# Optimization experiments

Hardware: AMD Instinct MI355X
Metric: run time of the kernel (lower is better)

The kernel has to match this reference:

```python
import jax, jax.numpy as jnp
import numpy as np

B, C, D, H, W = 4, 64, 32, 64, 64
CH = C // 2


def setup_inputs() -> dict:
    key = jax.random.key(0)
    ks = jax.random.split(key, 9)
    s = 0.05
    return {
        "x": jax.random.normal(ks[0], (B, C, D, H, W), dtype=jnp.float32),
        "wqr": jax.random.normal(ks[1], (1, C), dtype=jnp.float32) * s,
        "wvr": jax.random.normal(ks[2], (CH, C), dtype=jnp.float32) * s,
        "wup": jax.random.normal(ks[3], (C, CH), dtype=jnp.float32) * s,
        "wql": jax.random.normal(ks[4], (CH, C), dtype=jnp.float32) * s,
        "wvl": jax.random.normal(ks[5], (CH, C), dtype=jnp.float32) * s,
        "wsk1": jax.random.normal(ks[6], (CH, C), dtype=jnp.float32) * s,
        "wsk2": jax.random.normal(ks[7], (C, CH), dtype=jnp.float32) * s,
        "wres": jax.random.normal(ks[8], (C, C), dtype=jnp.float32) * s,
    }


def reference(x, wqr, wvr, wup, wql, wvl, wsk1, wsk2, wres):
    b, c, d, h, w = x.shape
    ch = c // 2
    n = d * h * w
    xf = x.reshape(b, c, n)
    # 1x1x1 conv (bias=False) + default mmcv ReLU activation
    conv = lambda Wt, t: jax.nn.relu(jnp.einsum('oc,bcn->bon', Wt, t))

    # ---- spatial (GCNet-style) branch ----
    input_x = conv(wvr, xf)                              # [b,ch,n]
    mask = jax.nn.softmax(conv(wqr, xf)[:, 0], axis=-1)  # [b,n]
    context = jnp.einsum('bcn,bn->bc', input_x, mask)    # [b,ch]
    mu = context.mean(-1, keepdims=True)
    var = context.var(-1, keepdims=True)                 # biased, like F.layer_norm
    ln = (context - mu) / jnp.sqrt(var + 1e-5)
    # conv_up with HSigmoid(bias=3, divisor=6)
    spatial_attn = jnp.clip((jnp.einsum('oc,bc->bo', wup, ln) + 3.0) / 6.0, 0.0, 1.0)  # [b,c]

    # ---- channel branch ----
    g_x = conv(wql, xf)                                  # [b,ch,n]
    avg_x = jax.nn.softmax(g_x.mean(-1), axis=-1)        # [b,ch]
    theta_x = conv(wvl, xf)                              # [b,ch,n]
    channel_attn = jax.nn.sigmoid(jnp.einsum('bc,bcn->bn', avg_x, theta_x))  # [b,n]

    # ---- recombination ----
    sequence = spatial_attn[:, :, None] * channel_attn[:, None, :]           # [b,c,n]
    parallel = jax.nn.softmax(channel_attn[:, None, :] + spatial_attn[:, :, None], axis=-1)

    # ---- SK gating ----
    u = (sequence + parallel).mean(-1)                   # global avg pool -> [b,c]
    a = jax.nn.relu(jnp.einsum('oc,bc->bo', wsk1, u))    # [b,ch]
    a = jax.nn.relu(jnp.einsum('oc,bc->bo', wsk2, a))    # [b,c]
    a = jax.nn.softmax(a, axis=-1)                       # softmax over channels
    sk = sequence * a[:, :, None] + parallel * (1.0 - a[:, :, None])  # [b,c,n]

    # ---- with_self=True path ----
    out = sk.sum(-1)[:, :, None] + conv(wres, xf)        # [b,c,n]
    return out.reshape(b, c, d, h, w)
```

## Files before the change

### kernel.cpp

```cpp
#include <hip/hip_runtime.h>

#define NB 4
#define NC 64
#define NCH 32
#define NPIX 131072

#define O_SUME 0
#define O_CTX  8
#define O_QL   136
#define O_SCA  264
#define O_SA   272
#define O_AVGX 528
#define O_K    656
#define O_WT1  1024
#define WT1_S  68
#define O_WT3  6144
#define O_WT5  8192
#define AF1_OFF 4096u
#define AF3_OFF 14336u
#define AF5_OFF 18432u
#define PB_OFF  32768u
#define PB_F    8192
#define XT_OFF  327680u
#define WS_NEED 67436544u

typedef short bf16x8 __attribute__((ext_vector_type(8)));
typedef float f32x4  __attribute__((ext_vector_type(4)));
typedef unsigned short u16x8 __attribute__((ext_vector_type(8)));

__device__ __forceinline__ float wave_sum64(float v) {
#pragma unroll
    for (int m = 32; m; m >>= 1) v += __shfl_xor(v, m, 64);
    return v;
}
__device__ __forceinline__ float gsum16(float v) {
#pragma unroll
    for (int m = 8; m; m >>= 1) v += __shfl_xor(v, m, 64);
    return v;
}
__device__ __forceinline__ unsigned short f2bf(float f) {
    unsigned u = __float_as_uint(f);
    u += 0x7FFFu + ((u >> 16) & 1u);
    return (unsigned short)(u >> 16);
}


__global__ __launch_bounds__(256) void k_T(
    const float* __restrict__ x, unsigned short* __restrict__ xt,
    const float* __restrict__ wqr, const float* __restrict__ wvr,
    const float* __restrict__ wql, const float* __restrict__ wvl,
    const float* __restrict__ wres, float* __restrict__ ws) {
    if (blockIdx.x == 0 && blockIdx.y == 0) {
        unsigned short* af1 = (unsigned short*)((char*)ws + AF1_OFF);
        unsigned short* af3 = (unsigned short*)((char*)ws + AF3_OFF);
        unsigned short* af5 = (unsigned short*)((char*)ws + AF5_OFF);
        for (int idx = threadIdx.x; idx < 5 * 2 * 64 * 8; idx += 256) {
            int j = idx & 7, lane = (idx >> 3) & 63, s = (idx >> 9) & 1, t = idx >> 10;
            int row = lane & 15, kg = lane >> 4, c = s * 32 + kg * 8 + j;
            float v;
            if (t < 2)      v = wvr[(t * 16 + row) * NC + c];
            else if (t < 4) v = wql[((t - 2) * 16 + row) * NC + c];
            else            v = (row == 0) ? wqr[c] : 0.f;
            af1[idx] = f2bf(v);
        }
        for (int idx = threadIdx.x; idx < 2 * 2 * 64 * 8; idx += 256) {
            int j = idx & 7, lane = (idx >> 3) & 63, s = (idx >> 9) & 1, t = idx >> 10;
            int row = lane & 15, kg = lane >> 4, c = s * 32 + kg * 8 + j;
            af3[idx] = f2bf(wvl[(t * 16 + row) * NC + c]);
        }
        for (int idx = threadIdx.x; idx < 4 * 2 * 64 * 8; idx += 256) {
            int j = idx & 7, lane = (idx >> 3) & 63, s = (idx >> 9) & 1, t = idx >> 10;
            int row = lane & 15, kg = lane >> 4, c = s * 32 + kg * 8 + j;
            af5[idx] = f2bf(wres[(t * 16 + row) * NC + c]);
        }
    }
    const int b = blockIdx.y;
    const int n0 = blockIdx.x * 64;
    __shared__ float lds[64 * 65];
    const int t = threadIdx.x;
    const int c = t >> 2, q = t & 3;
    const float* src = x + (size_t)(b * NC + c) * NPIX + n0;
#pragma unroll
    for (int k = 0; k < 4; ++k) {
        float4 v = *(const float4*)(src + q * 4 + k * 16);
        lds[c * 65 + q * 4 + k * 16 + 0] = v.x;
        lds[c * 65 + q * 4 + k * 16 + 1] = v.y;
        lds[c * 65 + q * 4 + k * 16 + 2] = v.z;
        lds[c * 65 + q * 4 + k * 16 + 3] = v.w;
    }
    __syncthreads();
    const int nl = t >> 2, cq = t & 3;
    u16x8 o0, o1;
#pragma unroll
    for (int i = 0; i < 8; ++i) o0[i] = f2bf(lds[(cq * 16 + i) * 65 + nl]);
#pragma unroll
    for (int i = 0; i < 8; ++i) o1[i] = f2bf(lds[(cq * 16 + 8 + i) * 65 + nl]);
    unsigned short* dst = xt + ((size_t)b * NPIX + n0 + nl) * NC + cq * 16;
    *(u16x8*)(dst) = o0;
    *(u16x8*)(dst + 8) = o1;
}

#define TPW 8
__global__ __launch_bounds__(256) void k_p1(
    const unsigned short* __restrict__ xt, float* __restrict__ ws) {
    const int b = blockIdx.y;
    const int lane = threadIdx.x & 63;
    const int wid = blockIdx.x * 4 + (threadIdx.x >> 6);
    const int col = lane & 15, kg = lane >> 4;
    const unsigned short* af1 = (const unsigned short*)((const char*)ws + AF1_OFF);

    __shared__ float red[65];
    for (int i = threadIdx.x; i < 65; i += 256) red[i] = 0.f;
    __syncthreads();

    bf16x8 A[5][2];
#pragma unroll
    for (int t = 0; t < 5; ++t)
#pragma unroll
        for (int s = 0; s < 2; ++s)
            A[t][s] = *(const bf16x8*)(af1 + ((t * 2 + s) * 64 + lane) * 8);

    float ctx[8], qla[8];
#pragma unroll
    for (int i = 0; i < 8; ++i) { ctx[i] = 0.f; qla[i] = 0.f; }
    float acc_e = 0.f;

    for (int it = 0; it < TPW; ++it) {
        const int n0 = (wid * TPW + it) * 16;
        const unsigned short* xr = xt + ((size_t)b * NPIX + n0 + col) * NC + kg * 8;
        bf16x8 B0 = *(const bf16x8*)(xr);
        bf16x8 B1 = *(const bf16x8*)(xr + 32);

        f32x4 c6 = {0.f, 0.f, 0.f, 0.f};
        c6 = __builtin_amdgcn_mfma_f32_16x16x32_bf16(A[4][0], B0, c6, 0, 0, 0);
        c6 = __builtin_amdgcn_mfma_f32_16x16x32_bf16(A[4][1], B1, c6, 0, 0, 0);
        float e = __expf(fmaxf(c6[0], 0.f));
        e = __shfl(e, col, 64);
        acc_e += e;

        f32x4 c0 = {0.f, 0.f, 0.f, 0.f}, c1 = {0.f, 0.f, 0.f, 0.f};
        c0 = __builtin_amdgcn_mfma_f32_16x16x32_bf16(A[0][0], B0, c0, 0, 0, 0);
        c0 = __builtin_amdgcn_mfma_f32_16x16x32_bf16(A[0][1], B1, c0, 0, 0, 0);
        c1 = __builtin_amdgcn_mfma_f32_16x16x32_bf16(A[1][0], B0, c1, 0, 0, 0);
        c1 = __builtin_amdgcn_mfma_f32_16x16x32_bf16(A[1][1], B1, c1, 0, 0, 0);
#pragma unroll
        for (int r = 0; r < 4; ++r) {
            ctx[r]     += fmaxf(c0[r], 0.f) * e;
            ctx[4 + r] += fmaxf(c1[r], 0.f) * e;
        }
        c0 = f32x4{0.f, 0.f, 0.f, 0.f}; c1 = f32x4{0.f, 0.f, 0.f, 0.f};
        c0 = __builtin_amdgcn_mfma_f32_16x16x32_bf16(A[2][0], B0, c0, 0, 0, 0);
        c0 = __builtin_amdgcn_mfma_f32_16x16x32_bf16(A[2][1], B1, c0, 0, 0, 0);
        c1 = __builtin_amdgcn_mfma_f32_16x16x32_bf16(A[3][0], B0, c1, 0, 0, 0);
        c1 = __builtin_amdgcn_mfma_f32_16x16x32_bf16(A[3][1], B1, c1, 0, 0, 0);
#pragma unroll
        for (int r = 0; r < 4; ++r) {
            qla[r]     += fmaxf(c0[r], 0.f);
            qla[4 + r] += fmaxf(c1[r], 0.f);
        }
    }

    acc_e = wave_sum64(acc_e) * 0.25f;
    if (lane == 0) atomicAdd(&red[64], acc_e);
#pragma unroll
    for (int i = 0; i < 8; ++i) {
        float v = gsum16(ctx[i]);
        float q = gsum16(qla[i]);
        if (col == 0) {
            int ch = (i >> 2) * 16 + kg * 4 + (i & 3);
            atomicAdd(&red[ch], v);
            atomicAdd(&red[32 + ch], q);
        }
    }
    __syncthreads();
    float* pb = ws + PB_F;
    if (threadIdx.x < 65)
        pb[((size_t)b * 65 + threadIdx.x) * 256 + blockIdx.x] = red[threadIdx.x];
}

__global__ __launch_bounds__(256) void k_p2f(
    const float* __restrict__ wup, float* __restrict__ ws) {
    const int b = threadIdx.x >> 6;
    const int lane = threadIdx.x & 63;
    __shared__ float q_s[NB][65];
    __shared__ float ln_s[NB][NCH];
    if (threadIdx.x < NB) ws[O_SCA + threadIdx.x] = 0.f;
    const float* pb = ws + PB_F;
    {
        const float4* p = (const float4*)(pb + ((size_t)b * 65 + lane) * 256);
        float s = 0.f;
        for (int k = 0; k < 64; ++k) { float4 v = p[k]; s += v.x + v.y + v.z + v.w; }
        q_s[b][lane] = s;
        if (lane == 0) {
            const float4* pe = (const float4*)(pb + ((size_t)b * 65 + 64) * 256);
            float se = 0.f;
            for (int k = 0; k < 64; ++k) { float4 v = pe[k]; se += v.x + v.y + v.z + v.w; }
            q_s[b][64] = se;
        }
    }
    __syncthreads();

    float se = q_s[b][64];
    float ctx = (lane < NCH) ? (q_s[b][lane] / se) : 0.f;
    float v = ctx, v2 = ctx * ctx;
#pragma unroll
    for (int m = 16; m; m >>= 1) { v += __shfl_xor(v, m, 64); v2 += __shfl_xor(v2, m, 64); }
    float mu = v / (float)NCH;
    float var = v2 / (float)NCH - mu * mu;
    float lnv = (ctx - mu) * rsqrtf(var + 1e-5f);
    if (lane < NCH) ln_s[b][lane] = lnv;
    __syncthreads();
    float s = 0.f;
#pragma unroll
    for (int ch = 0; ch < NCH; ++ch) s = fmaf(wup[lane * NCH + ch], ln_s[b][ch], s);
    ws[O_SA + b * NC + lane] = fminf(fmaxf((s + 3.f) * (1.f / 6.f), 0.f), 1.f);
    if (lane < NCH) {
        float l = q_s[b][32 + lane] * (1.f / (float)NPIX);
        float mx = l;
#pragma unroll
        for (int m = 16; m; m >>= 1) mx = fmaxf(mx, __shfl_xor(mx, m, 64));
        float e = __expf(l - mx);
        float sm = e;
#pragma unroll
        for (int m = 16; m; m >>= 1) sm += __shfl_xor(sm, m, 64);
        ws[O_AVGX + b * NCH + lane] = e / sm;
    }
}

__global__ __launch_bounds__(256) void k_p3v(
    const unsigned short* __restrict__ xt, float* __restrict__ ws) {
    const int b = blockIdx.y;
    const int lane = threadIdx.x & 63;
    const int wid = blockIdx.x * 4 + (threadIdx.x >> 6);
    const int col = lane & 15, kg = lane >> 4;
    const unsigned short* af3 = (const unsigned short*)((const char*)ws + AF3_OFF);

    __shared__ float red;
    if (threadIdx.x == 0) red = 0.f;
    __syncthreads();

    bf16x8 A[2][2];
#pragma unroll
    for (int t = 0; t < 2; ++t)
#pragma unroll
        for (int s = 0; s < 2; ++s)
            A[t][s] = *(const bf16x8*)(af3 + ((t * 2 + s) * 64 + lane) * 8);
    float ax0[4], ax1[4];
#pragma unroll
    for (int r = 0; r < 4; ++r) {
        ax0[r] = ws[O_AVGX + b * NCH + kg * 4 + r];
        ax1[r] = ws[O_AVGX + b * NCH + 16 + kg * 4 + r];
    }

    float acc = 0.f;
    for (int it = 0; it < TPW; ++it) {
        const int n0 = (wid * TPW + it) * 16;
        const unsigned short* xr = xt + ((size_t)b * NPIX + n0 + col) * NC + kg * 8;
        bf16x8 B0 = *(const bf16x8*)(xr);
        bf16x8 B1 = *(const bf16x8*)(xr + 32);
        f32x4 c0 = {0.f, 0.f, 0.f, 0.f}, c1 = {0.f, 0.f, 0.f, 0.f};
        c0 = __builtin_amdgcn_mfma_f32_16x16x32_bf16(A[0][0], B0, c0, 0, 0, 0);
        c0 = __builtin_amdgcn_mfma_f32_16x16x32_bf16(A[0][1], B1, c0, 0, 0, 0);
        c1 = __builtin_amdgcn_mfma_f32_16x16x32_bf16(A[1][0], B0, c1, 0, 0, 0);
        c1 = __builtin_amdgcn_mfma_f32_16x16x32_bf16(A[1][1], B1, c1, 0, 0, 0);
        float sp = 0.f;
#pragma unroll
        for (int r = 0; r < 4; ++r) {
            sp = fmaf(ax0[r], fmaxf(c0[r], 0.f), sp);
            sp = fmaf(ax1[r], fmaxf(c1[r], 0.f), sp);
        }
        sp += __shfl_xor(sp, 16, 64);
        sp += __shfl_xor(sp, 32, 64);
        acc += 1.f / (1.f + __expf(-sp));
    }
    acc = wave_sum64(acc) * 0.25f;
    if (lane == 0) atomicAdd(&red, acc);
    __syncthreads();
    if (threadIdx.x == 0) atomicAdd(&ws[O_SCA + b], red);
}

__global__ __launch_bounds__(256) void k_p5(
    const unsigned short* __restrict__ xt, const float* __restrict__ ws,
    const float* __restrict__ wsk1, const float* __restrict__ wsk2,
    float* __restrict__ out) {
    const int b = blockIdx.y;
    const int tid = threadIdx.x;
    const int lane = tid & 63;
    const int wid = blockIdx.x * 4 + (tid >> 6);
    const int col = lane & 15, kg = lane >> 4;
    const unsigned short* af5 = (const unsigned short*)((const char*)ws + AF5_OFF);

    __shared__ float u_s[NC];
    __shared__ float a1_s[NCH];
    __shared__ float K_s[NC];

    const float invn = 1.f / (float)NPIX;
    if (tid < NC) {
        float sca = ws[O_SCA + b];
        float sa = ws[O_SA + b * NC + tid];
        u_s[tid] = fmaf(sa, sca * invn, invn);
    }
    __syncthreads();
    if (tid < NCH) {
        float s = 0.f;
#pragma unroll
        for (int c = 0; c < NC; ++c) s = fmaf(wsk1[tid * NC + c], u_s[c], s);
        a1_s[tid] = fmaxf(s, 0.f);
    }
    __syncthreads();
    if (tid < NC) {
        float s2 = 0.f;
#pragma unroll
        for (int ch = 0; ch < NCH; ++ch) s2 = fmaf(wsk2[tid * NCH + ch], a1_s[ch], s2);
        s2 = fmaxf(s2, 0.f);
        float mx = s2;
#pragma unroll
        for (int m = 32; m; m >>= 1) mx = fmaxf(mx, __shfl_xor(mx, m, 64));
        float e = __expf(s2 - mx);
        float sm = e;
#pragma unroll
        for (int m = 32; m; m >>= 1) sm += __shfl_xor(sm, m, 64);
        float a = e / sm;
        float sca = ws[O_SCA + b];
        float sa = ws[O_SA + b * NC + tid];
        K_s[tid] = fmaf(a, sa * sca, 1.f - a);
    }
    __syncthreads();

    bf16x8 A[4][2];
#pragma unroll
    for (int t = 0; t < 4; ++t)
#pragma unroll
        for (int s = 0; s < 2; ++s)
            A[t][s] = *(const bf16x8*)(af5 + ((t * 2 + s) * 64 + lane) * 8);
    float kv[4][4];
#pragma unroll
    for (int t = 0; t < 4; ++t)
#pragma unroll
        for (int r = 0; r < 4; ++r)
            kv[t][r] = K_s[t * 16 + kg * 4 + r];

    for (int it = 0; it < TPW; ++it) {
        const int n0 = (wid * TPW + it) * 16;
        const unsigned short* xr = xt + ((size_t)b * NPIX + n0 + col) * NC + kg * 8;
        bf16x8 B0 = *(const bf16x8*)(xr);
        bf16x8 B1 = *(const bf16x8*)(xr + 32);
#pragma unroll
        for (int t = 0; t < 4; ++t) {
            f32x4 c = {0.f, 0.f, 0.f, 0.f};
            c = __builtin_amdgcn_mfma_f32_16x16x32_bf16(A[t][0], B0, c, 0, 0, 0);
            c = __builtin_amdgcn_mfma_f32_16x16x32_bf16(A[t][1], B1, c, 0, 0, 0);
#pragma unroll
            for (int r = 0; r < 4; ++r) {
                int o = t * 16 + kg * 4 + r;
                out[((size_t)(b * NC + o)) * NPIX + n0 + col] = kv[t][r] + fmaxf(c[r], 0.f);
            }
        }
    }
}

__global__ __launch_bounds__(256) void k_prep(
    const float* __restrict__ wqr, const float* __restrict__ wvr,
    const float* __restrict__ wql, const float* __restrict__ wvl,
    const float* __restrict__ wres, float* __restrict__ ws) {
    for (int i = threadIdx.x; i < NC * WT1_S; i += 256) {
        int c = i / WT1_S, j = i % WT1_S;
        float v = 0.f;
        if (j == 0)       v = wqr[c];
        else if (j <= 32) v = wvr[(j - 1) * NC + c];
        else if (j <= 64) v = wql[(j - 33) * NC + c];
        ws[O_WT1 + i] = v;
    }
    for (int i = threadIdx.x; i < NC * NCH; i += 256) {
        int c = i / NCH, ch = i % NCH;
        ws[O_WT3 + i] = wvl[ch * NC + c];
    }
    for (int i = threadIdx.x; i < NC * NC; i += 256) {
        int c = i / NC, o = i % NC;
        ws[O_WT5 + i] = wres[o * NC + c];
    }
}

__global__ __launch_bounds__(256) void k_pass1(
    const float* __restrict__ x, float* __restrict__ ws) {
    const int b = blockIdx.y;
    const float* xb = x + (size_t)b * NC * NPIX;
    __shared__ float wlds[NC * WT1_S];
    __shared__ float red[1 + 2 * NCH];
    for (int i = threadIdx.x; i < NC * WT1_S; i += 256) wlds[i] = ws[O_WT1 + i];
    for (int i = threadIdx.x; i < 1 + 2 * NCH; i += 256) red[i] = 0.f;
    __syncthreads();
    const int n2 = blockIdx.x * 256 + threadIdx.x;
    float dqr0 = 0.f, dqr1 = 0.f;
    float dv[NCH][2], dq[NCH][2];
#pragma unroll
    for (int i = 0; i < NCH; ++i) { dv[i][0] = dv[i][1] = 0.f; dq[i][0] = dq[i][1] = 0.f; }
    for (int c = 0; c < NC; ++c) {
        const float2 xv = *(const float2*)(xb + (size_t)c * NPIX + 2 * n2);
        const float* wr = wlds + c * WT1_S;
        dqr0 = fmaf(wr[0], xv.x, dqr0);
        dqr1 = fmaf(wr[0], xv.y, dqr1);
#pragma unroll
        for (int ch = 0; ch < NCH; ++ch) {
            const float wv = wr[1 + ch], wq = wr[33 + ch];
            dv[ch][0] = fmaf(wv, xv.x, dv[ch][0]);
            dv[ch][1] = fmaf(wv, xv.y, dv[ch][1]);
            dq[ch][0] = fmaf(wq, xv.x, dq[ch][0]);
            dq[ch][1] = fmaf(wq, xv.y, dq[ch][1]);
        }
    }
    const float e0 = __expf(fmaxf(dqr0, 0.f));
    const float e1 = __expf(fmaxf(dqr1, 0.f));
    float acc_e = wave_sum64(e0 + e1);
    if ((threadIdx.x & 63) == 0) atomicAdd(&red[0], acc_e);
#pragma unroll
    for (int ch = 0; ch < NCH; ++ch) {
        float v = wave_sum64(fmaxf(dv[ch][0], 0.f) * e0 + fmaxf(dv[ch][1], 0.f) * e1);
        float q = wave_sum64(fmaxf(dq[ch][0], 0.f) + fmaxf(dq[ch][1], 0.f));
        if ((threadIdx.x & 63) == 0) { atomicAdd(&red[1 + ch], v); atomicAdd(&red[1 + NCH + ch], q); }
    }
    __syncthreads();
    if (threadIdx.x == 0) atomicAdd(&ws[O_SUME + b], red[0]);
    if (threadIdx.x < NCH) {
        atomicAdd(&ws[O_CTX + b * NCH + threadIdx.x], red[1 + threadIdx.x]);
        atomicAdd(&ws[O_QL  + b * NCH + threadIdx.x], red[1 + NCH + threadIdx.x]);
    }
}

__global__ __launch_bounds__(256) void k_pass2(
    const float* __restrict__ wup, float* __restrict__ ws) {
    const int b = threadIdx.x >> 6;
    const int lane = threadIdx.x & 63;
    __shared__ float ln_s[NB][NCH];
    float se = ws[O_SUME + b];
    float ctx = (lane < NCH) ? (ws[O_CTX + b * NCH + lane] / se) : 0.f;
    float v = ctx, v2 = ctx * ctx;
#pragma unroll
    for (int m = 16; m; m >>= 1) { v += __shfl_xor(v, m, 64); v2 += __shfl_xor(v2, m, 64); }
    float mu = v / (float)NCH;
    float var = v2 / (float)NCH - mu * mu;
    float lnv = (ctx - mu) * rsqrtf(var + 1e-5f);
    if (lane < NCH) ln_s[b][lane] = lnv;
    __syncthreads();
    float s = 0.f;
#pragma unroll
    for (int ch = 0; ch < NCH; ++ch) s = fmaf(wup[lane * NCH + ch], ln_s[b][ch], s);
    ws[O_SA + b * NC + lane] = fminf(fmaxf((s + 3.f) * (1.f / 6.f), 0.f), 1.f);
    if (lane < NCH) {
        float l = ws[O_QL + b * NCH + lane] * (1.f / (float)NPIX);
        float mx = l;
#pragma unroll
        for (int m = 16; m; m >>= 1) mx = fmaxf(mx, __shfl_xor(mx, m, 64));
        float e = __expf(l - mx);
        float sm = e;
#pragma unroll
        for (int m = 16; m; m >>= 1) sm += __shfl_xor(sm, m, 64);
        ws[O_AVGX + b * NCH + lane] = e / sm;
    }
}

__global__ __launch_bounds__(256) void k_pass3(
    const float* __restrict__ x, float* __restrict__ ws) {
    const int b = blockIdx.y;
    const float* xb = x + (size_t)b * NC * NPIX;
    __shared__ float wlds[NC * NCH];
    __shared__ float red;
    for (int i = threadIdx.x; i < NC * NCH; i += 256) wlds[i] = ws[O_WT3 + i];
    if (threadIdx.x == 0) red = 0.f;
    __syncthreads();
    const int n2 = blockIdx.x * 256 + threadIdx.x;
    float dv[NCH][2];
#pragma unroll
    for (int i = 0; i < NCH; ++i) dv[i][0] = dv[i][1] = 0.f;
    for (int c = 0; c < NC; ++c) {
        const float2 xv = *(const float2*)(xb + (size_t)c * NPIX + 2 * n2);
        const float* wr = wlds + c * NCH;
#pragma unroll
        for (int ch = 0; ch < NCH; ++ch) {
            dv[ch][0] = fmaf(wr[ch], xv.x, dv[ch][0]);
            dv[ch][1] = fmaf(wr[ch], xv.y, dv[ch][1]);
        }
    }
    float s0 = 0.f, s1 = 0.f;
#pragma unroll
    for (int ch = 0; ch < NCH; ++ch) {
        const float ax = ws[O_AVGX + b * NCH + ch];
        s0 = fmaf(ax, fmaxf(dv[ch][0], 0.f), s0);
        s1 = fmaf(ax, fmaxf(dv[ch][1], 0.f), s1);
    }
    float acc = wave_sum64(1.f / (1.f + __expf(-s0)) + 1.f / (1.f + __expf(-s1)));
    if ((threadIdx.x & 63) == 0) atomicAdd(&red, acc);
    __syncthreads();
    if (threadIdx.x == 0) atomicAdd(&ws[O_SCA + b], red);
}

__global__ __launch_bounds__(256) void k_pass4(
    const float* __restrict__ wsk1, const float* __restrict__ wsk2,
    float* __restrict__ ws) {
    const int b = threadIdx.x >> 6;
    const int lane = threadIdx.x & 63;
    __shared__ float u_s[NB][NC];
    __shared__ float a1_s[NB][NCH];
    float sca = ws[O_SCA + b];
    float sa = ws[O_SA + b * NC + lane];
    float invn = 1.f / (float)NPIX;
    u_s[b][lane] = fmaf(sa, sca * invn, invn);
    __syncthreads();
    if (lane < NCH) {
        float s = 0.f;
#pragma unroll
        for (int c = 0; c < NC; ++c) s = fmaf(wsk1[lane * NC + c], u_s[b][c], s);
        a1_s[b][lane] = fmaxf(s, 0.f);
    }
    __syncthreads();
    float s2 = 0.f;
#pragma unroll
    for (int ch = 0; ch < NCH; ++ch) s2 = fmaf(wsk2[lane * NCH + ch], a1_s[b][ch], s2);
    s2 = fmaxf(s2, 0.f);
    float mx = s2;
#pragma unroll
    for (int m = 32; m; m >>= 1) mx = fmaxf(mx, __shfl_xor(mx, m, 64));
    float e = __expf(s2 - mx);
    float sm = e;
#pragma unroll
    for (int m = 32; m; m >>= 1) sm += __shfl_xor(sm, m, 64);
    float a = e / sm;
    ws[O_K + b * NC + lane] = fmaf(a, sa * sca, 1.f - a);
}

__global__ __launch_bounds__(256) void k_pass5(
    const float* __restrict__ x, const float* __restrict__ ws,
    float* __restrict__ out) {
    const int b = blockIdx.y;
    const float* xb = x + (size_t)b * NC * NPIX;
    float* ob = out + (size_t)b * NC * NPIX;
    __shared__ float wlds[NC * NC];
    for (int i = threadIdx.x; i < NC * NC; i += 256) wlds[i] = ws[O_WT5 + i];
    __syncthreads();
    const int n2 = blockIdx.x * 256 + threadIdx.x;
    float acc[NC][2];
#pragma unroll
    for (int o = 0; o < NC; ++o) acc[o][0] = acc[o][1] = 0.f;
    for (int c = 0; c < NC; ++c) {
        const float2 xv = *(const float2*)(xb + (size_t)c * NPIX + 2 * n2);
        const float* wr = wlds + c * NC;
#pragma unroll
        for (int o = 0; o < NC; ++o) {
            acc[o][0] = fmaf(wr[o], xv.x, acc[o][0]);
            acc[o][1] = fmaf(wr[o], xv.y, acc[o][1]);
        }
    }
#pragma unroll
    for (int o = 0; o < NC; ++o) {
        const float k = ws[O_K + b * NC + o];
        float2 r;
        r.x = k + fmaxf(acc[o][0], 0.f);
        r.y = k + fmaxf(acc[o][1], 0.f);
        *(float2*)(ob + (size_t)o * NPIX + 2 * n2) = r;
    }
}

extern "C" void kernel_launch(void* const* d_in, const int* in_sizes, int n_in,
                              void* d_out, int out_size, void* d_ws, size_t ws_size,
                              hipStream_t stream) {
    const float* x    = (const float*)d_in[0];
    const float* wqr  = (const float*)d_in[1];
    const float* wvr  = (const float*)d_in[2];
    const float* wup  = (const float*)d_in[3];
    const float* wql  = (const float*)d_in[4];
    const float* wvl  = (const float*)d_in[5];
    const float* wsk1 = (const float*)d_in[6];
    const float* wsk2 = (const float*)d_in[7];
    const float* wres = (const float*)d_in[8];
    float* out = (float*)d_out;
    float* ws  = (float*)d_ws;

    dim3 blk(256);

    if (ws_size >= (size_t)WS_NEED) {
        unsigned short* xt = (unsigned short*)((char*)d_ws + XT_OFF);
        k_T<<<dim3(NPIX / 64, NB), blk, 0, stream>>>(x, xt, wqr, wvr, wql, wvl, wres, ws);
        k_p1<<<dim3(NPIX / (16 * 4 * TPW), NB), blk, 0, stream>>>(xt, ws);
        k_p2f<<<dim3(1), blk, 0, stream>>>(wup, ws);
        k_p3v<<<dim3(NPIX / (16 * 4 * TPW), NB), blk, 0, stream>>>(xt, ws);
        k_p5<<<dim3(NPIX / (16 * 4 * TPW), NB), blk, 0, stream>>>(xt, ws, wsk1, wsk2, out);
    } else {
        hipMemsetAsync(d_ws, 0, 272 * sizeof(float), stream);
        k_prep<<<dim3(1), blk, 0, stream>>>(wqr, wvr, wql, wvl, wres, ws);
        dim3 g(NPIX / (2 * 256), NB);
        k_pass1<<<g, blk, 0, stream>>>(x, ws);
        k_pass2<<<dim3(1), blk, 0, stream>>>(wup, ws);
        k_pass3<<<g, blk, 0, stream>>>(x, ws);
        k_pass4<<<dim3(1), blk, 0, stream>>>(wsk1, wsk2, ws);
        k_pass5<<<g, blk, 0, stream>>>(x, ws, out);
    }
}
```

Baseline: 147.1 us.

## Fuse transpose with first statistics pass and transpose final MFMA output

Merges the fp32-to-bf16 transpose kernel with the first reduction pass, so the statistics MMAs read the tile straight from LDS instead of re-reading the transposed copy from global memory. Per-block partials go to a larger buffer that a new parallel reduction kernel sums before the small finalize kernel. The final residual-conv kernel swaps the MFMA operands so each lane writes a float4 along pixels rather than scattered scalar stores. In exchange, the fused kernel loads weights from global memory in every block and the partial buffer grows.

```diff
diff --git a/kernel.cpp b/kernel.cpp
--- a/kernel.cpp
+++ b/kernel.cpp
@@ -16,13 +16,13 @@
 #define WT1_S  68
 #define O_WT3  6144
 #define O_WT5  8192
-#define AF1_OFF 4096u
 #define AF3_OFF 14336u
 #define AF5_OFF 18432u
 #define PB_OFF  32768u
 #define PB_F    8192
-#define XT_OFF  327680u
-#define WS_NEED 67436544u
+#define NBLK    2048
+#define XT_OFF  2162688u
+#define WS_NEED 69271552u
 
 typedef short bf16x8 __attribute__((ext_vector_type(8)));
 typedef float f32x4  __attribute__((ext_vector_type(4)));
@@ -43,41 +43,45 @@
     u += 0x7FFFu + ((u >> 16) & 1u);
     return (unsigned short)(u >> 16);
 }
-
-
-__global__ __launch_bounds__(256) void k_T(
+__device__ __forceinline__ bf16x8 ld8f(const float* p) {
+    float4 a = *(const float4*)p;
+    float4 c = *(const float4*)(p + 4);
+    bf16x8 r;
+    r[0] = (short)f2bf(a.x); r[1] = (short)f2bf(a.y);
+    r[2] = (short)f2bf(a.z); r[3] = (short)f2bf(a.w);
+    r[4] = (short)f2bf(c.x); r[5] = (short)f2bf(c.y);
+    r[6] = (short)f2bf(c.z); r[7] = (short)f2bf(c.w);
+    return r;
+}
+
+
+__global__ __launch_bounds__(256) void k_Tp1(
     const float* __restrict__ x, unsigned short* __restrict__ xt,
     const float* __restrict__ wqr, const float* __restrict__ wvr,
     const float* __restrict__ wql, const float* __restrict__ wvl,
     const float* __restrict__ wres, float* __restrict__ ws) {
-    if (blockIdx.x == 0 && blockIdx.y == 0) {
-        unsigned short* af1 = (unsigned short*)((char*)ws + AF1_OFF);
+    const int b = blockIdx.y;
+    const int n0 = blockIdx.x * 64;
+    const int t = threadIdx.x;
+    __shared__ float lds[64 * 65];
+    __shared__ float red[65];
+
+    if (blockIdx.x == 0 && b == 0) {
         unsigned short* af3 = (unsigned short*)((char*)ws + AF3_OFF);
         unsigned short* af5 = (unsigned short*)((char*)ws + AF5_OFF);
-        for (int idx = threadIdx.x; idx < 5 * 2 * 64 * 8; idx += 256) {
-            int j = idx & 7, lane = (idx >> 3) & 63, s = (idx >> 9) & 1, t = idx >> 10;
+        for (int idx = t; idx < 2 * 2 * 64 * 8; idx += 256) {
+            int j = idx & 7, lane = (idx >> 3) & 63, s = (idx >> 9) & 1, tt = idx >> 10;
             int row = lane & 15, kg = lane >> 4, c = s * 32 + kg * 8 + j;
-            float v;
-            if (t < 2)      v = wvr[(t * 16 + row) * NC + c];
-            else if (t < 4) v = wql[((t - 2) * 16 + row) * NC + c];
-            else            v = (row == 0) ? wqr[c] : 0.f;
-            af1[idx] = f2bf(v);
-        }
-        for (int idx = threadIdx.x; idx < 2 * 2 * 64 * 8; idx += 256) {
-            int j = idx & 7, lane = (idx >> 3) & 63, s = (idx >> 9) & 1, t = idx >> 10;
+            af3[idx] = f2bf(wvl[(tt * 16 + row) * NC + c]);
+        }
+        for (int idx = t; idx < 4 * 2 * 64 * 8; idx += 256) {
+            int j = idx & 7, lane = (idx >> 3) & 63, s = (idx >> 9) & 1, tt = idx >> 10;
             int row = lane & 15, kg = lane >> 4, c = s * 32 + kg * 8 + j;
-            af3[idx] = f2bf(wvl[(t * 16 + row) * NC + c]);
-        }
-        for (int idx = threadIdx.x; idx < 4 * 2 * 64 * 8; idx += 256) {
-            int j = idx & 7, lane = (idx >> 3) & 63, s = (idx >> 9) & 1, t = idx >> 10;
-            int row = lane & 15, kg = lane >> 4, c = s * 32 + kg * 8 + j;
-            af5[idx] = f2bf(wres[(t * 16 + row) * NC + c]);
-        }
-    }
-    const int b = blockIdx.y;
-    const int n0 = blockIdx.x * 64;
-    __shared__ float lds[64 * 65];
-    const int t = threadIdx.x;
+            af5[idx] = f2bf(wres[(tt * 16 + row) * NC + c]);
+        }
+    }
+    for (int i = t; i < 65; i += 256) red[i] = 0.f;
+
     const int c = t >> 2, q = t & 3;
     const float* src = x + (size_t)(b * NC + c) * NPIX + n0;
 #pragma unroll
@@ -89,144 +93,110 @@
         lds[c * 65 + q * 4 + k * 16 + 3] = v.w;
     }
     __syncthreads();
+
     const int nl = t >> 2, cq = t & 3;
-    u16x8 o0, o1;
-#pragma unroll
-    for (int i = 0; i < 8; ++i) o0[i] = f2bf(lds[(cq * 16 + i) * 65 + nl]);
-#pragma unroll
-    for (int i = 0; i < 8; ++i) o1[i] = f2bf(lds[(cq * 16 + 8 + i) * 65 + nl]);
-    unsigned short* dst = xt + ((size_t)b * NPIX + n0 + nl) * NC + cq * 16;
-    *(u16x8*)(dst) = o0;
-    *(u16x8*)(dst + 8) = o1;
-}
-
-#define TPW 8
-__global__ __launch_bounds__(256) void k_p1(
-    const unsigned short* __restrict__ xt, float* __restrict__ ws) {
-    const int b = blockIdx.y;
-    const int lane = threadIdx.x & 63;
-    const int wid = blockIdx.x * 4 + (threadIdx.x >> 6);
+    {
+        u16x8 o0, o1;
+#pragma unroll
+        for (int i = 0; i < 8; ++i) o0[i] = f2bf(lds[(cq * 16 + i) * 65 + nl]);
+#pragma unroll
+        for (int i = 0; i < 8; ++i) o1[i] = f2bf(lds[(cq * 16 + 8 + i) * 65 + nl]);
+        unsigned short* dst = xt + ((size_t)b * NPIX + n0 + nl) * NC + cq * 16;
+        *(u16x8*)(dst) = o0;
+        *(u16x8*)(dst + 8) = o1;
+    }
+
+    const int lane = t & 63, w = t >> 6;
     const int col = lane & 15, kg = lane >> 4;
-    const unsigned short* af1 = (const unsigned short*)((const char*)ws + AF1_OFF);
-
-    __shared__ float red[65];
-    for (int i = threadIdx.x; i < 65; i += 256) red[i] = 0.f;
-    __syncthreads();
-
-    bf16x8 A[5][2];
-#pragma unroll
-    for (int t = 0; t < 5; ++t)
-#pragma unroll
-        for (int s = 0; s < 2; ++s)
-            A[t][s] = *(const bf16x8*)(af1 + ((t * 2 + s) * 64 + lane) * 8);
-
-    float ctx[8], qla[8];
-#pragma unroll
-    for (int i = 0; i < 8; ++i) { ctx[i] = 0.f; qla[i] = 0.f; }
-    float acc_e = 0.f;
-
-    for (int it = 0; it < TPW; ++it) {
-        const int n0 = (wid * TPW + it) * 16;
-        const unsigned short* xr = xt + ((size_t)b * NPIX + n0 + col) * NC + kg * 8;
-        bf16x8 B0 = *(const bf16x8*)(xr);
-        bf16x8 B1 = *(const bf16x8*)(xr + 32);
-
-        f32x4 c6 = {0.f, 0.f, 0.f, 0.f};
-        c6 = __builtin_amdgcn_mfma_f32_16x16x32_bf16(A[4][0], B0, c6, 0, 0, 0);
-        c6 = __builtin_amdgcn_mfma_f32_16x16x32_bf16(A[4][1], B1, c6, 0, 0, 0);
-        float e = __expf(fmaxf(c6[0], 0.f));
-        e = __shfl(e, col, 64);
-        acc_e += e;
-
-        f32x4 c0 = {0.f, 0.f, 0.f, 0.f}, c1 = {0.f, 0.f, 0.f, 0.f};
-        c0 = __builtin_amdgcn_mfma_f32_16x16x32_bf16(A[0][0], B0, c0, 0, 0, 0);
-        c0 = __builtin_amdgcn_mfma_f32_16x16x32_bf16(A[0][1], B1, c0, 0, 0, 0);
-        c1 = __builtin_amdgcn_mfma_f32_16x16x32_bf16(A[1][0], B0, c1, 0, 0, 0);
-        c1 = __builtin_amdgcn_mfma_f32_16x16x32_bf16(A[1][1], B1, c1, 0, 0, 0);
-#pragma unroll
-        for (int r = 0; r < 4; ++r) {
-            ctx[r]     += fmaxf(c0[r], 0.f) * e;
-            ctx[4 + r] += fmaxf(c1[r], 0.f) * e;
-        }
-        c0 = f32x4{0.f, 0.f, 0.f, 0.f}; c1 = f32x4{0.f, 0.f, 0.f, 0.f};
-        c0 = __builtin_amdgcn_mfma_f32_16x16x32_bf16(A[2][0], B0, c0, 0, 0, 0);
-        c0 = __builtin_amdgcn_mfma_f32_16x16x32_bf16(A[2][1], B1, c0, 0, 0, 0);
-        c1 = __builtin_amdgcn_mfma_f32_16x16x32_bf16(A[3][0], B0, c1, 0, 0, 0);
-        c1 = __builtin_amdgcn_mfma_f32_16x16x32_bf16(A[3][1], B1, c1, 0, 0, 0);
-#pragma unroll
-        for (int r = 0; r < 4; ++r) {
-            qla[r]     += fmaxf(c0[r], 0.f);
-            qla[4 + r] += fmaxf(c1[r], 0.f);
-        }
-    }
-
-    acc_e = wave_sum64(acc_e) * 0.25f;
+    const int px = w * 16 + col;
+
+    bf16x8 B0, B1;
+#pragma unroll
+    for (int j = 0; j < 8; ++j) B0[j] = (short)f2bf(lds[(kg * 8 + j) * 65 + px]);
+#pragma unroll
+    for (int j = 0; j < 8; ++j) B1[j] = (short)f2bf(lds[(32 + kg * 8 + j) * 65 + px]);
+
+    bf16x8 A0[2], A1[2], A2[2], A3[2], Aq[2];
+#pragma unroll
+    for (int s = 0; s < 2; ++s) {
+        A0[s] = ld8f(wvr + (col) * NC + s * 32 + kg * 8);
+        A1[s] = ld8f(wvr + (16 + col) * NC + s * 32 + kg * 8);
+        A2[s] = ld8f(wql + (col) * NC + s * 32 + kg * 8);
+        A3[s] = ld8f(wql + (16 + col) * NC + s * 32 + kg * 8);
+    }
+    if (col == 0) {
+#pragma unroll
+        for (int s = 0; s < 2; ++s) Aq[s] = ld8f(wqr + s * 32 + kg * 8);
+    } else {
+        bf16x8 z = {0, 0, 0, 0, 0, 0, 0, 0};
+        Aq[0] = z; Aq[1] = z;
+    }
+
+    f32x4 c6 = {0.f, 0.f, 0.f, 0.f};
+    c6 = __builtin_amdgcn_mfma_f32_16x16x32_bf16(Aq[0], B0, c6, 0, 0, 0);
+    c6 = __builtin_amdgcn_mfma_f32_16x16x32_bf16(Aq[1], B1, c6, 0, 0, 0);
+    float e = __expf(fmaxf(c6[0], 0.f));
+    e = __shfl(e, col, 64);
+    float acc_e = wave_sum64(e) * 0.25f;
     if (lane == 0) atomicAdd(&red[64], acc_e);
+
+    f32x4 c0 = {0.f, 0.f, 0.f, 0.f}, c1 = {0.f, 0.f, 0.f, 0.f};
+    c0 = __builtin_amdgcn_mfma_f32_16x16x32_bf16(A0[0], B0, c0, 0, 0, 0);
+    c0 = __builtin_amdgcn_mfma_f32_16x16x32_bf16(A0[1], B1, c0, 0, 0, 0);
+    c1 = __builtin_amdgcn_mfma_f32_16x16x32_bf16(A1[0], B0, c1, 0, 0, 0);
+    c1 = __builtin_amdgcn_mfma_f32_16x16x32_bf16(A1[1], B1, c1, 0, 0, 0);
+    float ctx[8];
+#pragma unroll
+    for (int r = 0; r < 4; ++r) {
+        ctx[r]     = fmaxf(c0[r], 0.f) * e;
+        ctx[4 + r] = fmaxf(c1[r], 0.f) * e;
+    }
+    c0 = f32x4{0.f, 0.f, 0.f, 0.f}; c1 = f32x4{0.f, 0.f, 0.f, 0.f};
+    c0 = __builtin_amdgcn_mfma_f32_16x16x32_bf16(A2[0], B0, c0, 0, 0, 0);
+    c0 = __builtin_amdgcn_mfma_f32_16x16x32_bf16(A2[1], B1, c0, 0, 0, 0);
+    c1 = __builtin_amdgcn_mfma_f32_16x16x32_bf16(A3[0], B0, c1, 0, 0, 0);
+    c1 = __builtin_amdgcn_mfma_f32_16x16x32_bf16(A3[1], B1, c1, 0, 0, 0);
+    float qla[8];
+#pragma unroll
+    for (int r = 0; r < 4; ++r) {
+        qla[r]     = fmaxf(c0[r], 0.f);
+        qla[4 + r] = fmaxf(c1[r], 0.f);
+    }
 #pragma unroll
     for (int i = 0; i < 8; ++i) {
         float v = gsum16(ctx[i]);
-        float q = gsum16(qla[i]);
+        float qv = gsum16(qla[i]);
         if (col == 0) {
             int ch = (i >> 2) * 16 + kg * 4 + (i & 3);
             atomicAdd(&red[ch], v);
-            atomicAdd(&red[32 + ch], q);
+            atomicAdd(&red[32 + ch], qv);
         }
     }
     __syncthreads();
     float* pb = ws + PB_F;
-    if (threadIdx.x < 65)
-        pb[((size_t)b * 65 + threadIdx.x) * 256 + blockIdx.x] = red[threadIdx.x];
-}
-
-__global__ __launch_bounds__(256) void k_p2f(
-    const float* __restrict__ wup, float* __restrict__ ws) {
-    const int b = threadIdx.x >> 6;
-    const int lane = threadIdx.x & 63;
-    __shared__ float q_s[NB][65];
-    __shared__ float ln_s[NB][NCH];
-    if (threadIdx.x < NB) ws[O_SCA + threadIdx.x] = 0.f;
-    const float* pb = ws + PB_F;
-    {
-        const float4* p = (const float4*)(pb + ((size_t)b * 65 + lane) * 256);
-        float s = 0.f;
-        for (int k = 0; k < 64; ++k) { float4 v = p[k]; s += v.x + v.y + v.z + v.w; }
-        q_s[b][lane] = s;
-        if (lane == 0) {
-            const float4* pe = (const float4*)(pb + ((size_t)b * 65 + 64) * 256);
-            float se = 0.f;
-            for (int k = 0; k < 64; ++k) { float4 v = pe[k]; se += v.x + v.y + v.z + v.w; }
-            q_s[b][64] = se;
-        }
-    }
-    __syncthreads();
-
-    float se = q_s[b][64];
-    float ctx = (lane < NCH) ? (q_s[b][lane] / se) : 0.f;
-    float v = ctx, v2 = ctx * ctx;
-#pragma unroll
-    for (int m = 16; m; m >>= 1) { v += __shfl_xor(v, m, 64); v2 += __shfl_xor(v2, m, 64); }
-    float mu = v / (float)NCH;
-    float var = v2 / (float)NCH - mu * mu;
-    float lnv = (ctx - mu) * rsqrtf(var + 1e-5f);
-    if (lane < NCH) ln_s[b][lane] = lnv;
-    __syncthreads();
+    if (t < 65)
+        pb[((size_t)b * 65 + t) * NBLK + blockIdx.x] = red[t];
+}
+
+__global__ __launch_bounds__(256) void k_red(float* __restrict__ ws) {
+    const int slot = blockIdx.x;
+    const int b = blockIdx.y;
+    const float* p = ws + PB_F + ((size_t)b * 65 + slot) * NBLK;
     float s = 0.f;
-#pragma unroll
-    for (int ch = 0; ch < NCH; ++ch) s = fmaf(wup[lane * NCH + ch], ln_s[b][ch], s);
-    ws[O_SA + b * NC + lane] = fminf(fmaxf((s + 3.f) * (1.f / 6.f), 0.f), 1.f);
-    if (lane < NCH) {
-        float l = q_s[b][32 + lane] * (1.f / (float)NPIX);
-        float mx = l;
-#pragma unroll
-        for (int m = 16; m; m >>= 1) mx = fmaxf(mx, __shfl_xor(mx, m, 64));
-        float e = __expf(l - mx);
-        float sm = e;
-#pragma unroll
-        for (int m = 16; m; m >>= 1) sm += __shfl_xor(sm, m, 64);
-        ws[O_AVGX + b * NCH + lane] = e / sm;
-    }
-}
-
+    for (int i = threadIdx.x; i < NBLK; i += 256) s += p[i];
+    s = wave_sum64(s);
+    __shared__ float r4[4];
+    if ((threadIdx.x & 63) == 0) r4[threadIdx.x >> 6] = s;
+    __syncthreads();
+    if (threadIdx.x == 0) {
+        float tot = r4[0] + r4[1] + r4[2] + r4[3];
+        if (slot < 32)      ws[O_CTX + b * NCH + slot] = tot;
+        else if (slot < 64) ws[O_QL + b * NCH + (slot - 32)] = tot;
+        else { ws[O_SUME + b] = tot; ws[O_SCA + b] = 0.f; }
+    }
+}
+
+#define TPW 8
 __global__ __launch_bounds__(256) void k_p3v(
     const unsigned short* __restrict__ xt, float* __restrict__ ws) {
     const int b = blockIdx.y;
@@ -333,12 +303,9 @@
 #pragma unroll
         for (int s = 0; s < 2; ++s)
             A[t][s] = *(const bf16x8*)(af5 + ((t * 2 + s) * 64 + lane) * 8);
-    float kv[4][4];
-#pragma unroll
-    for (int t = 0; t < 4; ++t)
-#pragma unroll
-        for (int r = 0; r < 4; ++r)
-            kv[t][r] = K_s[t * 16 + kg * 4 + r];
+    float kvc[4];
+#pragma unroll
+    for (int t = 0; t < 4; ++t) kvc[t] = K_s[t * 16 + col];
 
     for (int it = 0; it < TPW; ++it) {
         const int n0 = (wid * TPW + it) * 16;
@@ -347,16 +314,83 @@
         bf16x8 B1 = *(const bf16x8*)(xr + 32);
 #pragma unroll
         for (int t = 0; t < 4; ++t) {
-            f32x4 c = {0.f, 0.f, 0.f, 0.f};
-            c = __builtin_amdgcn_mfma_f32_16x16x32_bf16(A[t][0], B0, c, 0, 0, 0);
-            c = __builtin_amdgcn_mfma_f32_16x16x32_bf16(A[t][1], B1, c, 0, 0, 0);
-#pragma unroll
-            for (int r = 0; r < 4; ++r) {
-                int o = t * 16 + kg * 4 + r;
-                out[((size_t)(b * NC + o)) * NPIX + n0 + col] = kv[t][r] + fmaxf(c[r], 0.f);
-            }
-        }
-    }
+            f32x4 cc = {0.f, 0.f, 0.f, 0.f};
+            cc = __builtin_amdgcn_mfma_f32_16x16x32_bf16(B0, A[t][0], cc, 0, 0, 0);
+            cc = __builtin_amdgcn_mfma_f32_16x16x32_bf16(B1, A[t][1], cc, 0, 0, 0);
+            float4 r;
+            r.x = kvc[t] + fmaxf(cc[0], 0.f);
+            r.y = kvc[t] + fmaxf(cc[1], 0.f);
+            r.z = kvc[t] + fmaxf(cc[2], 0.f);
+            r.w = kvc[t] + fmaxf(cc[3], 0.f);
+            *(float4*)(out + ((size_t)(b * NC + t * 16 + col)) * NPIX + n0 + kg * 4) = r;
+        }
+    }
+}
+
+__global__ __launch_bounds__(256) void k_pass2(
+    const float* __restrict__ wup, float* __restrict__ ws) {
+    const int b = threadIdx.x >> 6;
+    const int lane = threadIdx.x & 63;
+    __shared__ float ln_s[NB][NCH];
+    float se = ws[O_SUME + b];
+    float ctx = (lane < NCH) ? (ws[O_CTX + b * NCH + lane] / se) : 0.f;
+    float v = ctx, v2 = ctx * ctx;
+#pragma unroll
+    for (int m = 16; m; m >>= 1) { v += __shfl_xor(v, m, 64); v2 += __shfl_xor(v2, m, 64); }
+    float mu = v / (float)NCH;
+    float var = v2 / (float)NCH - mu * mu;
+    float lnv = (ctx - mu) * rsqrtf(var + 1e-5f);
+    if (lane < NCH) ln_s[b][lane] = lnv;
+    __syncthreads();
+    float s = 0.f;
+#pragma unroll
+    for (int ch = 0; ch < NCH; ++ch) s = fmaf(wup[lane * NCH + ch], ln_s[b][ch], s);
+    ws[O_SA + b * NC + lane] = fminf(fmaxf((s + 3.f) * (1.f / 6.f), 0.f), 1.f);
+    if (lane < NCH) {
+        float l = ws[O_QL + b * NCH + lane] * (1.f / (float)NPIX);
+        float mx = l;
+#pragma unroll
+        for (int m = 16; m; m >>= 1) mx = fmaxf(mx, __shfl_xor(mx, m, 64));
+        float e = __expf(l - mx);
+        float sm = e;
+#pragma unroll
+        for (int m = 16; m; m >>= 1) sm += __shfl_xor(sm, m, 64);
+        ws[O_AVGX + b * NCH + lane] = e / sm;
+    }
+}
+
+__global__ __launch_bounds__(256) void k_pass4(
+    const float* __restrict__ wsk1, const float* __restrict__ wsk2,
+    float* __restrict__ ws) {
+    const int b = threadIdx.x >> 6;
+    const int lane = threadIdx.x & 63;
+    __shared__ float u_s[NB][NC];
+    __shared__ float a1_s[NB][NCH];
+    float sca = ws[O_SCA + b];
+    float sa = ws[O_SA + b * NC + lane];
+    float invn = 1.f / (float)NPIX;
+    u_s[b][lane] = fmaf(sa, sca * invn, invn);
+    __syncthreads();
+    if (lane < NCH) {
+        float s = 0.f;
+#pragma unroll
+        for (int c = 0; c < NC; ++c) s = fmaf(wsk1[lane * NC + c], u_s[b][c], s);
+        a1_s[b][lane] = fmaxf(s, 0.f);
+    }
+    __syncthreads();
+    float s2 = 0.f;
+#pragma unroll
+    for (int ch = 0; ch < NCH; ++ch) s2 = fmaf(wsk2[lane * NCH + ch], a1_s[b][ch], s2);
+    s2 = fmaxf(s2, 0.f);
+    float mx = s2;
+#pragma unroll
+    for (int m = 32; m; m >>= 1) mx = fmaxf(mx, __shfl_xor(mx, m, 64));
+    float e = __expf(s2 - mx);
+    float sm = e;
+#pragma unroll
+    for (int m = 32; m; m >>= 1) sm += __shfl_xor(sm, m, 64);
+    float a = e / sm;
+    ws[O_K + b * NC + lane] = fmaf(a, sa * sca, 1.f - a);
 }
 
 __global__ __launch_bounds__(256) void k_prep(
@@ -427,38 +461,6 @@
     }
 }
 
-__global__ __launch_bounds__(256) void k_pass2(
-    const float* __restrict__ wup, float* __restrict__ ws) {
-    const int b = threadIdx.x >> 6;
-    const int lane = threadIdx.x & 63;
-    __shared__ float ln_s[NB][NCH];
-    float se = ws[O_SUME + b];
-    float ctx = (lane < NCH) ? (ws[O_CTX + b * NCH + lane] / se) : 0.f;
-    float v = ctx, v2 = ctx * ctx;
-#pragma unroll
-    for (int m = 16; m; m >>= 1) { v += __shfl_xor(v, m, 64); v2 += __shfl_xor(v2, m, 64); }
-    float mu = v / (float)NCH;
-    float var = v2 / (float)NCH - mu * mu;
-    float lnv = (ctx - mu) * rsqrtf(var + 1e-5f);
-    if (lane < NCH) ln_s[b][lane] = lnv;
-    __syncthreads();
-    float s = 0.f;
-#pragma unroll
-    for (int ch = 0; ch < NCH; ++ch) s = fmaf(wup[lane * NCH + ch], ln_s[b][ch], s);
-    ws[O_SA + b * NC + lane] = fminf(fmaxf((s + 3.f) * (1.f / 6.f), 0.f), 1.f);
-    if (lane < NCH) {
-        float l = ws[O_QL + b * NCH + lane] * (1.f / (float)NPIX);
-        float mx = l;
-#pragma unroll
-        for (int m = 16; m; m >>= 1) mx = fmaxf(mx, __shfl_xor(mx, m, 64));
-        float e = __expf(l - mx);
-        float sm = e;
-#pragma unroll
-        for (int m = 16; m; m >>= 1) sm += __shfl_xor(sm, m, 64);
-        ws[O_AVGX + b * NCH + lane] = e / sm;
-    }
-}
-
 __global__ __launch_bounds__(256) void k_pass3(
     const float* __restrict__ x, float* __restrict__ ws) {
     const int b = blockIdx.y;
@@ -492,40 +494,6 @@
     if ((threadIdx.x & 63) == 0) atomicAdd(&red, acc);
     __syncthreads();
     if (threadIdx.x == 0) atomicAdd(&ws[O_SCA + b], red);
-}
-
-__global__ __launch_bounds__(256) void k_pass4(
-    const float* __restrict__ wsk1, const float* __restrict__ wsk2,
-    float* __restrict__ ws) {
-    const int b = threadIdx.x >> 6;
-    const int lane = threadIdx.x & 63;
-    __shared__ float u_s[NB][NC];
-    __shared__ float a1_s[NB][NCH];
-    float sca = ws[O_SCA + b];
-    float sa = ws[O_SA + b * NC + lane];
-    float invn = 1.f / (float)NPIX;
-    u_s[b][lane] = fmaf(sa, sca * invn, invn);
-    __syncthreads();
-    if (lane < NCH) {
-        float s = 0.f;
-#pragma unroll
-        for (int c = 0; c < NC; ++c) s = fmaf(wsk1[lane * NC + c], u_s[b][c], s);
-        a1_s[b][lane] = fmaxf(s, 0.f);
-    }
-    __syncthreads();
-    float s2 = 0.f;
-#pragma unroll
-    for (int ch = 0; ch < NCH; ++ch) s2 = fmaf(wsk2[lane * NCH + ch], a1_s[b][ch], s2);
-    s2 = fmaxf(s2, 0.f);
-    float mx = s2;
-#pragma unroll
-    for (int m = 32; m; m >>= 1) mx = fmaxf(mx, __shfl_xor(mx, m, 64));
-    float e = __expf(s2 - mx);
-    float sm = e;
-#pragma unroll
-    for (int m = 32; m; m >>= 1) sm += __shfl_xor(sm, m, 64);
-    float a = e / sm;
-    ws[O_K + b * NC + lane] = fmaf(a, sa * sca, 1.f - a);
 }
 
 __global__ __launch_bounds__(256) void k_pass5(
@@ -579,9 +547,9 @@
 
     if (ws_size >= (size_t)WS_NEED) {
         unsigned short* xt = (unsigned short*)((char*)d_ws + XT_OFF);
-        k_T<<<dim3(NPIX / 64, NB), blk, 0, stream>>>(x, xt, wqr, wvr, wql, wvl, wres, ws);
-        k_p1<<<dim3(NPIX / (16 * 4 * TPW), NB), blk, 0, stream>>>(xt, ws);
-        k_p2f<<<dim3(1), blk, 0, stream>>>(wup, ws);
+        k_Tp1<<<dim3(NBLK, NB), blk, 0, stream>>>(x, xt, wqr, wvr, wql, wvl, wres, ws);
+        k_red<<<dim3(65, NB), blk, 0, stream>>>(ws);
+        k_pass2<<<dim3(1), blk, 0, stream>>>(wup, ws);
         k_p3v<<<dim3(NPIX / (16 * 4 * TPW), NB), blk, 0, stream>>>(xt, ws);
         k_p5<<<dim3(NPIX / (16 * 4 * TPW), NB), blk, 0, stream>>>(xt, ws, wsk1, wsk2, out);
     } else {
```

New measurement: 168.9 us. 1.15x slower.

## Vectorize final output stores via swapped MFMA operands and parallelize partial reductions

Applied to the files above, without the earlier changes.

In the final output kernel, the MFMA operands are swapped so each lane holds four consecutive pixels of one output channel, which allows a single float4 store instead of four strided scalar stores. The serial single-block partial-sum reduction (k_p2f) is split into a 65×NB-block reduction kernel followed by the existing k_pass2 finalization. The aim is to cut write-coalescing cost on the large output and the latency of the one-block reduction, at the cost of one extra kernel launch. k_p1's grid is now hardcoded to NPBLK=256, which must still match NPIX/(64*TPW).

```diff
diff --git a/kernel.cpp b/kernel.cpp
--- a/kernel.cpp
+++ b/kernel.cpp
@@ -21,6 +21,7 @@
 #define AF5_OFF 18432u
 #define PB_OFF  32768u
 #define PB_F    8192
+#define NPBLK   256
 #define XT_OFF  327680u
 #define WS_NEED 67436544u
 
@@ -175,55 +176,23 @@
     __syncthreads();
     float* pb = ws + PB_F;
     if (threadIdx.x < 65)
-        pb[((size_t)b * 65 + threadIdx.x) * 256 + blockIdx.x] = red[threadIdx.x];
-}
-
-__global__ __launch_bounds__(256) void k_p2f(
-    const float* __restrict__ wup, float* __restrict__ ws) {
-    const int b = threadIdx.x >> 6;
-    const int lane = threadIdx.x & 63;
-    __shared__ float q_s[NB][65];
-    __shared__ float ln_s[NB][NCH];
-    if (threadIdx.x < NB) ws[O_SCA + threadIdx.x] = 0.f;
-    const float* pb = ws + PB_F;
-    {
-        const float4* p = (const float4*)(pb + ((size_t)b * 65 + lane) * 256);
-        float s = 0.f;
-        for (int k = 0; k < 64; ++k) { float4 v = p[k]; s += v.x + v.y + v.z + v.w; }
-        q_s[b][lane] = s;
-        if (lane == 0) {
-            const float4* pe = (const float4*)(pb + ((size_t)b * 65 + 64) * 256);
-            float se = 0.f;
-            for (int k = 0; k < 64; ++k) { float4 v = pe[k]; se += v.x + v.y + v.z + v.w; }
-            q_s[b][64] = se;
-        }
-    }
-    __syncthreads();
-
-    float se = q_s[b][64];
-    float ctx = (lane < NCH) ? (q_s[b][lane] / se) : 0.f;
-    float v = ctx, v2 = ctx * ctx;
-#pragma unroll
-    for (int m = 16; m; m >>= 1) { v += __shfl_xor(v, m, 64); v2 += __shfl_xor(v2, m, 64); }
-    float mu = v / (float)NCH;
-    float var = v2 / (float)NCH - mu * mu;
-    float lnv = (ctx - mu) * rsqrtf(var + 1e-5f);
-    if (lane < NCH) ln_s[b][lane] = lnv;
-    __syncthreads();
-    float s = 0.f;
-#pragma unroll
-    for (int ch = 0; ch < NCH; ++ch) s = fmaf(wup[lane * NCH + ch], ln_s[b][ch], s);
-    ws[O_SA + b * NC + lane] = fminf(fmaxf((s + 3.f) * (1.f / 6.f), 0.f), 1.f);
-    if (lane < NCH) {
-        float l = q_s[b][32 + lane] * (1.f / (float)NPIX);
-        float mx = l;
-#pragma unroll
-        for (int m = 16; m; m >>= 1) mx = fmaxf(mx, __shfl_xor(mx, m, 64));
-        float e = __expf(l - mx);
-        float sm = e;
-#pragma unroll
-        for (int m = 16; m; m >>= 1) sm += __shfl_xor(sm, m, 64);
-        ws[O_AVGX + b * NCH + lane] = e / sm;
+        pb[((size_t)b * 65 + threadIdx.x) * NPBLK + blockIdx.x] = red[threadIdx.x];
+}
+
+__global__ __launch_bounds__(256) void k_red(float* __restrict__ ws) {
+    const int slot = blockIdx.x;
+    const int b = blockIdx.y;
+    const float* p = ws + PB_F + ((size_t)b * 65 + slot) * NPBLK;
+    float s = (threadIdx.x < NPBLK) ? p[threadIdx.x] : 0.f;
+    s = wave_sum64(s);
+    __shared__ float r4[4];
+    if ((threadIdx.x & 63) == 0) r4[threadIdx.x >> 6] = s;
+    __syncthreads();
+    if (threadIdx.x == 0) {
+        float tot = r4[0] + r4[1] + r4[2] + r4[3];
+        if (slot < 32)      ws[O_CTX + b * NCH + slot] = tot;
+        else if (slot < 64) ws[O_QL + b * NCH + (slot - 32)] = tot;
+        else { ws[O_SUME + b] = tot; ws[O_SCA + b] = 0.f; }
     }
 }
 
@@ -333,12 +302,9 @@
 #pragma unroll
         for (int s = 0; s < 2; ++s)
             A[t][s] = *(const bf16x8*)(af5 + ((t * 2 + s) * 64 + lane) * 8);
-    float kv[4][4];
-#pragma unroll
-    for (int t = 0; t < 4; ++t)
-#pragma unroll
-        for (int r = 0; r < 4; ++r)
-            kv[t][r] = K_s[t * 16 + kg * 4 + r];
+    float kvc[4];
+#pragma unroll
+    for (int t = 0; t < 4; ++t) kvc[t] = K_s[t * 16 + col];
 
     for (int it = 0; it < TPW; ++it) {
         const int n0 = (wid * TPW + it) * 16;
@@ -347,15 +313,48 @@
         bf16x8 B1 = *(const bf16x8*)(xr + 32);
 #pragma unroll
         for (int t = 0; t < 4; ++t) {
-            f32x4 c = {0.f, 0.f, 0.f, 0.f};
-            c = __builtin_amdgcn_mfma_f32_16x16x32_bf16(A[t][0], B0, c, 0, 0, 0);
-            c = __builtin_amdgcn_mfma_f32_16x16x32_bf16(A[t][1], B1, c, 0, 0, 0);
-#pragma unroll
-            for (int r = 0; r < 4; ++r) {
-                int o = t * 16 + kg * 4 + r;
-                out[((size_t)(b * NC + o)) * NPIX + n0 + col] = kv[t][r] + fmaxf(c[r], 0.f);
-            }
-        }
+            f32x4 cc = {0.f, 0.f, 0.f, 0.f};
+            cc = __builtin_amdgcn_mfma_f32_16x16x32_bf16(B0, A[t][0], cc, 0, 0, 0);
+            cc = __builtin_amdgcn_mfma_f32_16x16x32_bf16(B1, A[t][1], cc, 0, 0, 0);
+            float4 r;
+            r.x = kvc[t] + fmaxf(cc[0], 0.f);
+            r.y = kvc[t] + fmaxf(cc[1], 0.f);
+            r.z = kvc[t] + fmaxf(cc[2], 0.f);
+            r.w = kvc[t] + fmaxf(cc[3], 0.f);
+            *(float4*)(out + ((size_t)(b * NC + t * 16 + col)) * NPIX + n0 + kg * 4) = r;
+        }
+    }
+}
+
+__global__ __launch_bounds__(256) void k_pass2(
+    const float* __restrict__ wup, float* __restrict__ ws) {
+    const int b = threadIdx.x >> 6;
+    const int lane = threadIdx.x & 63;
+    __shared__ float ln_s[NB][NCH];
+    float se = ws[O_SUME + b];
+    float ctx = (lane < NCH) ? (ws[O_CTX + b * NCH + lane] / se) : 0.f;
+    float v = ctx, v2 = ctx * ctx;
+#pragma unroll
+    for (int m = 16; m; m >>= 1) { v += __shfl_xor(v, m, 64); v2 += __shfl_xor(v2, m, 64); }
+    float mu = v / (float)NCH;
+    float var = v2 / (float)NCH - mu * mu;
+    float lnv = (ctx - mu) * rsqrtf(var + 1e-5f);
+    if (lane < NCH) ln_s[b][lane] = lnv;
+    __syncthreads();
+    float s = 0.f;
+#pragma unroll
+    for (int ch = 0; ch < NCH; ++ch) s = fmaf(wup[lane * NCH + ch], ln_s[b][ch], s);
+    ws[O_SA + b * NC + lane] = fminf(fmaxf((s + 3.f) * (1.f / 6.f), 0.f), 1.f);
+    if (lane < NCH) {
+        float l = ws[O_QL + b * NCH + lane] * (1.f / (float)NPIX);
+        float mx = l;
+#pragma unroll
+        for (int m = 16; m; m >>= 1) mx = fmaxf(mx, __shfl_xor(mx, m, 64));
+        float e = __expf(l - mx);
+        float sm = e;
+#pragma unroll
+        for (int m = 16; m; m >>= 1) sm += __shfl_xor(sm, m, 64);
+        ws[O_AVGX + b * NCH + lane] = e / sm;
     }
 }
 
@@ -424,38 +423,6 @@
     if (threadIdx.x < NCH) {
         atomicAdd(&ws[O_CTX + b * NCH + threadIdx.x], red[1 + threadIdx.x]);
         atomicAdd(&ws[O_QL  + b * NCH + threadIdx.x], red[1 + NCH + threadIdx.x]);
-    }
-}
-
-__global__ __launch_bounds__(256) void k_pass2(
-    const float* __restrict__ wup, float* __restrict__ ws) {
-    const int b = threadIdx.x >> 6;
-    const int lane = threadIdx.x & 63;
-    __shared__ float ln_s[NB][NCH];
-    float se = ws[O_SUME + b];
-    float ctx = (lane < NCH) ? (ws[O_CTX + b * NCH + lane] / se) : 0.f;
-    float v = ctx, v2 = ctx * ctx;
-#pragma unroll
-    for (int m = 16; m; m >>= 1) { v += __shfl_xor(v, m, 64); v2 += __shfl_xor(v2, m, 64); }
-    float mu = v / (float)NCH;
-    float var = v2 / (float)NCH - mu * mu;
-    float lnv = (ctx - mu) * rsqrtf(var + 1e-5f);
-    if (lane < NCH) ln_s[b][lane] = lnv;
-    __syncthreads();
-    float s = 0.f;
-#pragma unroll
-    for (int ch = 0; ch < NCH; ++ch) s = fmaf(wup[lane * NCH + ch], ln_s[b][ch], s);
-    ws[O_SA + b * NC + lane] = fminf(fmaxf((s + 3.f) * (1.f / 6.f), 0.f), 1.f);
-    if (lane < NCH) {
-        float l = ws[O_QL + b * NCH + lane] * (1.f / (float)NPIX);
-        float mx = l;
-#pragma unroll
-        for (int m = 16; m; m >>= 1) mx = fmaxf(mx, __shfl_xor(mx, m, 64));
-        float e = __expf(l - mx);
-        float sm = e;
-#pragma unroll
-        for (int m = 16; m; m >>= 1) sm += __shfl_xor(sm, m, 64);
-        ws[O_AVGX + b * NCH + lane] = e / sm;
     }
 }
 
@@ -580,8 +547,9 @@
     if (ws_size >= (size_t)WS_NEED) {
         unsigned short* xt = (unsigned short*)((char*)d_ws + XT_OFF);
         k_T<<<dim3(NPIX / 64, NB), blk, 0, stream>>>(x, xt, wqr, wvr, wql, wvl, wres, ws);
-        k_p1<<<dim3(NPIX / (16 * 4 * TPW), NB), blk, 0, stream>>>(xt, ws);
-        k_p2f<<<dim3(1), blk, 0, stream>>>(wup, ws);
+        k_p1<<<dim3(NPBLK, NB), blk, 0, stream>>>(xt, ws);
+        k_red<<<dim3(65, NB), blk, 0, stream>>>(ws);
+        k_pass2<<<dim3(1), blk, 0, stream>>>(wup, ws);
         k_p3v<<<dim3(NPIX / (16 * 4 * TPW), NB), blk, 0, stream>>>(xt, ws);
         k_p5<<<dim3(NPIX / (16 * 4 * TPW), NB), blk, 0, stream>>>(xt, ws, wsk1, wsk2, out);
     } else {
```

Measured after the change: 139.0 us. 5.5% less time.
